# Optimization experiments

Measured on AMD Instinct MI355X. Metric: run time of the kernel, lower is better.

Reference implementation:

```python
import jax, jax.numpy as jnp
import numpy as np

N = 4            # polynomial nodes per segment
SEGMENTS = 32
IN_F = 1024
OUT_F = 1024
BATCH = 32
LENGTH = 2.0
HALF = 0.5 * LENGTH
K = (N - 1) * SEGMENTS + 1  # 97 coefficients per (out,in) pair


def setup_inputs() -> dict:
    key = jax.random.key(0)
    k1, k2 = jax.random.split(key)
    x = jax.random.uniform(k1, (BATCH, IN_F), jnp.float32, -1.0, 1.0)
    wm = 1.0 / IN_F  # uniform_(-weight_magnitude/in_features, +...)
    w = jax.random.uniform(k2, (OUT_F, IN_F, K), jnp.float32, -wm, wm)
    return {"x": x, "w": w}


def _lagrange_basis(x):
    # Chebyshev-Lobatto nodes on [-1, 1]: X_k = -cos(k*pi/(n-1))
    X = -jnp.cos(jnp.arange(N) * (np.pi / (N - 1))).astype(x.dtype)
    eye = jnp.eye(N, dtype=bool)
    D = jnp.where(eye, 1.0, X[:, None] - X[None, :])      # X[j] - X[m], diag -> 1
    diff = x[..., None, None] - X                          # [..., 1, n(m)]
    ratio = jnp.where(eye, 1.0, diff / D)                  # [..., n(j), n(m)]
    return jnp.prod(ratio, axis=-1)                        # [..., n] basis_j(x)


def reference(x, w):
    # segment index per element, clamped to [0, segments-1]
    id_min = jnp.clip(((x + HALF) / LENGTH * SEGMENTS).astype(jnp.int32), 0, SEGMENTS - 1)
    id_max = id_min + 1
    wid_min = id_min * (N - 1)                             # [B, I]
    idx = wid_min[..., None] + jnp.arange(N, dtype=jnp.int32)  # [B, I, n]
    # gather per-element coefficient windows: wsel[b,i,o,j] = w[o,i,idx[b,i,j]]
    w2 = jnp.transpose(w, (1, 0, 2))                       # [I, O, K]
    wsel = jnp.take_along_axis(w2[None], idx[:, :, None, :], axis=3)  # [B, I, O, n]
    # map x into local segment coordinates on [-half, half]
    x_min = 2.0 * id_min.astype(x.dtype) / SEGMENTS - 1.0
    x_max = 2.0 * id_max.astype(x.dtype) / SEGMENTS - 1.0
    x_in = LENGTH * (x - x_min) / (x_max - x_min) - HALF   # [B, I]
    basis = _lagrange_basis(x_in)                          # [B, I, n]
    # sum over in_features and nodes: 'ijk,jkli->jl' in the original repo
    return jnp.einsum('bin,bion->bo', basis, wsel)
```

## Files before the change

### kernel.cpp

```cpp
#include <hip/hip_runtime.h>

#define IN_F   1024
#define OUT_F  1024
#define KCOEF  97
#define CROWS  32
#define CFL    (CROWS * KCOEF)
#define CB     (CFL * 4)
#define NCH    32

typedef float f4 __attribute__((ext_vector_type(4)));

#define AS1 __attribute__((address_space(1)))
#define AS3 __attribute__((address_space(3)))

__global__ __launch_bounds__(256)
void pack_x(const float* __restrict__ x, float* __restrict__ xq) {
    int t = blockIdx.x * 256 + threadIdx.x;
    int b = t >> 10, i = t & 1023;
    xq[((i >> 2) << 7) + (b << 2) + (i & 3)] = x[t];
}

#define ISSUE_W(c, buf_) do {                                                   \
    const char* _gw = wbase + (size_t)(c) * CB;                                 \
    char* _lw = (char*)&shw[buf_][0];                                           \
    _Pragma("unroll")                                                           \
    for (int _k = 0; _k < 3; ++_k)                                              \
        __builtin_amdgcn_global_load_lds(                                       \
            (const AS1 void*)(_gw + (_k << 12) + (t << 4)),                     \
            (AS3 void*)(_lw + (_k << 12) + (wv << 10)), 16, 0, 0);              \
    if (lane < 2)                                                               \
        __builtin_amdgcn_global_load_lds(                                       \
            (const AS1 void*)(_gw + 12288 + (wv << 5) + (lane << 4)),           \
            (AS3 void*)(_lw + 12288 + (wv << 5)), 16, 0, 0);                    \
} while (0)

#define XLOAD(c) (*(const f4*)&xq[((((c) << 3) + g) << 7) + (b << 2)])

#define BASIS(b_, j_, xv_) do {                                           \
    _Pragma("unroll")                                                     \
    for (int _r = 0; _r < 4; ++_r) {                                      \
        float _x = xv_[_r];                                               \
        float _s = (_x + 1.0f) * 16.0f;                                   \
        int _id = (int)_s;                                                \
        _id = _id < 0 ? 0 : (_id > 31 ? 31 : _id);                        \
        float _d  = _x - ((float)_id * 0.0625f - 1.0f);                   \
        float _tt = fmaf(_d, 32.0f, -1.0f);                               \
        float _ap = _tt + 1.0f, _bp = _tt + 0.5f;                         \
        float _cm = _tt - 0.5f, _dm = _tt - 1.0f;                         \
        float _uu = _bp * _cm, _vv = _ap * _dm;                           \
        b_[_r][0] = _uu * _dm * (-2.0f / 3.0f);                           \
        b_[_r][1] = _vv * _cm * ( 4.0f / 3.0f);                           \
        b_[_r][2] = _vv * _bp * (-4.0f / 3.0f);                           \
        b_[_r][3] = _uu * _ap * ( 2.0f / 3.0f);                           \
        j_[_r] = _id * 3;                                                 \
    }                                                                     \
} while (0)

#define COMPUTE(b_, j_, buf_) do {                                        \
    const float* _rows = &shw[buf_][(g << 2) * KCOEF];                    \
    _Pragma("unroll")                                                     \
    for (int _r = 0; _r < 4; ++_r) {                                      \
        const float* _row = _rows + _r * KCOEF;                           \
        int _j = j_[_r];                                                  \
        float _w0 = _row[_j], _w1 = _row[_j + 1];                         \
        float _w2 = _row[_j + 2], _w3 = _row[_j + 3];                     \
        float _v = fmaf(b_[_r][0], _w0, fmaf(b_[_r][1], _w1,              \
                   fmaf(b_[_r][2], _w2, b_[_r][3] * _w3)));               \
        if (_r & 1) acc1 += _v; else acc0 += _v;                          \
    }                                                                     \
} while (0)

#define SBAR0() __builtin_amdgcn_sched_barrier(0)

#define WAITBAR(N) do {                                                   \
    asm volatile("s_waitcnt vmcnt(" #N ")" ::: "memory");                 \
    SBAR0();                                                              \
    __builtin_amdgcn_s_barrier();                                         \
    SBAR0();                                                              \
} while (0)

#define ENDBAR() do {                                                     \
    SBAR0();                                                              \
    __builtin_amdgcn_s_barrier();                                         \
    SBAR0();                                                              \
} while (0)

__global__ __launch_bounds__(256, 4)
void piecewise_main(const float* __restrict__ xq,
                    const float* __restrict__ w,
                    float* __restrict__ out) {
    const int bid = blockIdx.x;
    const int o = (bid & 7) * 128 + (bid >> 3);
    const int t    = threadIdx.x;
    const int wv   = t >> 6;
    const int lane = t & 63;
    const int g    = t >> 5;
    const int b    = t & 31;

    __shared__ __align__(16) float shw[3][CFL];
    __shared__ float red[256];

    const char* wbase = (const char*)(w + (size_t)o * (IN_F * KCOEF));

    float bA[4][4], bB[4][4];
    int   jA[4],   jB[4];
    float acc0 = 0.f, acc1 = 0.f;

    f4 xv0 = XLOAD(0);
    SBAR0();
    ISSUE_W(0, 0);
    ISSUE_W(1, 1);
    BASIS(bA, jA, xv0);

    for (int cc = 0; cc < 30; cc += 2) {
        const int p0 = cc % 3, p1 = (cc + 1) % 3, p2 = (cc + 2) % 3;
        f4 xv1 = XLOAD(cc + 1);
        SBAR0();
        ISSUE_W(cc + 2, p2);
        WAITBAR(4);
        BASIS(bB, jB, xv1);
        COMPUTE(bA, jA, p0);
        ENDBAR();
        f4 xv2 = XLOAD(cc + 2);
        SBAR0();
        ISSUE_W(cc + 3, p0);
        WAITBAR(4);
        BASIS(bA, jA, xv2);
        COMPUTE(bB, jB, p1);
        ENDBAR();
    }

    f4 xv31 = XLOAD(31);
    asm volatile("s_waitcnt vmcnt(0)" ::: "memory");
    SBAR0();
    __builtin_amdgcn_s_barrier();
    SBAR0();
    BASIS(bB, jB, xv31);
    COMPUTE(bA, jA, 0);
    COMPUTE(bB, jB, 1);

    red[t] = acc0 + acc1;
    __syncthreads();
    if (t < 32) {
        float sum = red[t];
        #pragma unroll
        for (int gg = 1; gg < 8; ++gg) sum += red[gg * 32 + t];
        out[t * OUT_F + o] = sum;
    }
}

extern "C" void kernel_launch(void* const* d_in, const int* in_sizes, int n_in,
                              void* d_out, int out_size, void* d_ws, size_t ws_size,
                              hipStream_t stream) {
    const float* x = (const float*)d_in[0];
    const float* w = (const float*)d_in[1];
    float*       out = (float*)d_out;
    float*       xq  = (float*)d_ws;

    pack_x<<<(32 * IN_F) / 256, 256, 0, stream>>>(x, xq);
    piecewise_main<<<OUT_F, 256, 0, stream>>>(xq, w, out);
}
```

Before: 80.72 us.

## Fuse x packing into main kernel and drop per-chunk end barrier

Removes the separate pack_x kernel and reads x directly from its row-major layout inside the main kernel, saving a launch and a workspace round trip. The triple-buffer loop is restructured with rotating LDS pointers and a single barrier per chunk instead of two, overlapping the next basis computation with outstanding loads. The direct x reads are less coalesced than the packed layout, and the single-barrier schedule depends on the vmcnt accounting being correct to avoid LDS races.

```diff
diff --git a/kernel.cpp b/kernel.cpp
--- a/kernel.cpp
+++ b/kernel.cpp
@@ -6,35 +6,28 @@
 #define CROWS  32
 #define CFL    (CROWS * KCOEF)
 #define CB     (CFL * 4)
-#define NCH    32
 
 typedef float f4 __attribute__((ext_vector_type(4)));
 
 #define AS1 __attribute__((address_space(1)))
 #define AS3 __attribute__((address_space(3)))
 
-__global__ __launch_bounds__(256)
-void pack_x(const float* __restrict__ x, float* __restrict__ xq) {
-    int t = blockIdx.x * 256 + threadIdx.x;
-    int b = t >> 10, i = t & 1023;
-    xq[((i >> 2) << 7) + (b << 2) + (i & 3)] = x[t];
-}
+#define SBAR0() __builtin_amdgcn_sched_barrier(0)
 
-#define ISSUE_W(c, buf_) do {                                                   \
-    const char* _gw = wbase + (size_t)(c) * CB;                                 \
-    char* _lw = (char*)&shw[buf_][0];                                           \
+#define ISSUE_W(c, lbuf) do {                                                   \
+    const char* _g = wbase + (size_t)(c) * CB;                                  \
     _Pragma("unroll")                                                           \
     for (int _k = 0; _k < 3; ++_k)                                              \
         __builtin_amdgcn_global_load_lds(                                       \
-            (const AS1 void*)(_gw + (_k << 12) + (t << 4)),                     \
-            (AS3 void*)(_lw + (_k << 12) + (wv << 10)), 16, 0, 0);              \
+            (const AS1 void*)(_g + (_k << 12) + (t << 4)),                      \
+            (AS3 void*)((lbuf) + (_k << 12) + (wv << 10)), 16, 0, 0);           \
     if (lane < 2)                                                               \
         __builtin_amdgcn_global_load_lds(                                       \
-            (const AS1 void*)(_gw + 12288 + (wv << 5) + (lane << 4)),           \
-            (AS3 void*)(_lw + 12288 + (wv << 5)), 16, 0, 0);                    \
+            (const AS1 void*)(_g + 12288 + (wv << 5) + (lane << 4)),            \
+            (AS3 void*)((lbuf) + 12288 + (wv << 5)), 16, 0, 0);                 \
 } while (0)
 
-#define XLOAD(c) (*(const f4*)&xq[((((c) << 3) + g) << 7) + (b << 2)])
+#define XLOAD(c) (*(const f4*)&xrow[((c) << 5) + (g << 2)])
 
 #define BASIS(b_, j_, xv_) do {                                           \
     _Pragma("unroll")                                                     \
@@ -56,8 +49,8 @@
     }                                                                     \
 } while (0)
 
-#define COMPUTE(b_, j_, buf_) do {                                        \
-    const float* _rows = &shw[buf_][(g << 2) * KCOEF];                    \
+#define COMPUTE(b_, j_, q_) do {                                          \
+    const float* _rows = (const float*)(q_) + (g << 2) * KCOEF;           \
     _Pragma("unroll")                                                     \
     for (int _r = 0; _r < 4; ++_r) {                                      \
         const float* _row = _rows + _r * KCOEF;                           \
@@ -70,8 +63,6 @@
     }                                                                     \
 } while (0)
 
-#define SBAR0() __builtin_amdgcn_sched_barrier(0)
-
 #define WAITBAR(N) do {                                                   \
     asm volatile("s_waitcnt vmcnt(" #N ")" ::: "memory");                 \
     SBAR0();                                                              \
@@ -79,16 +70,10 @@
     SBAR0();                                                              \
 } while (0)
 
-#define ENDBAR() do {                                                     \
-    SBAR0();                                                              \
-    __builtin_amdgcn_s_barrier();                                         \
-    SBAR0();                                                              \
-} while (0)
-
 __global__ __launch_bounds__(256, 4)
-void piecewise_main(const float* __restrict__ xq,
-                    const float* __restrict__ w,
-                    float* __restrict__ out) {
+void piecewise_fused(const float* __restrict__ x,
+                     const float* __restrict__ w,
+                     float* __restrict__ out) {
     const int bid = blockIdx.x;
     const int o = (bid & 7) * 128 + (bid >> 3);
     const int t    = threadIdx.x;
@@ -100,44 +85,46 @@
     __shared__ __align__(16) float shw[3][CFL];
     __shared__ float red[256];
 
-    const char* wbase = (const char*)(w + (size_t)o * (IN_F * KCOEF));
+    const char*  wbase = (const char*)(w + (size_t)o * (IN_F * KCOEF));
+    const float* xrow  = x + b * IN_F;
+
+    char* q0 = (char*)&shw[0][0];
+    char* q1 = (char*)&shw[1][0];
+    char* q2 = (char*)&shw[2][0];
 
     float bA[4][4], bB[4][4];
     int   jA[4],   jB[4];
+    f4 xvA, xvB;
     float acc0 = 0.f, acc1 = 0.f;
 
-    f4 xv0 = XLOAD(0);
-    SBAR0();
-    ISSUE_W(0, 0);
-    ISSUE_W(1, 1);
-    BASIS(bA, jA, xv0);
+    xvA = XLOAD(0);
+    BASIS(bA, jA, xvA);
+    ISSUE_W(0, q0);
+    xvB = XLOAD(1);
+    ISSUE_W(1, q1);
 
     for (int cc = 0; cc < 30; cc += 2) {
-        const int p0 = cc % 3, p1 = (cc + 1) % 3, p2 = (cc + 2) % 3;
-        f4 xv1 = XLOAD(cc + 1);
+        WAITBAR(6);
+        xvA = XLOAD(cc + 2);
+        ISSUE_W(cc + 2, q2);
+        COMPUTE(bA, jA, q0);
         SBAR0();
-        ISSUE_W(cc + 2, p2);
-        WAITBAR(4);
-        BASIS(bB, jB, xv1);
-        COMPUTE(bA, jA, p0);
-        ENDBAR();
-        f4 xv2 = XLOAD(cc + 2);
+        BASIS(bB, jB, xvB);
+        WAITBAR(6);
+        xvB = XLOAD(cc + 3);
+        ISSUE_W(cc + 3, q0);
+        COMPUTE(bB, jB, q1);
         SBAR0();
-        ISSUE_W(cc + 3, p0);
-        WAITBAR(4);
-        BASIS(bA, jA, xv2);
-        COMPUTE(bB, jB, p1);
-        ENDBAR();
+        BASIS(bA, jA, xvA);
+        char* tmp = q0; q0 = q2; q2 = q1; q1 = tmp;
     }
 
-    f4 xv31 = XLOAD(31);
-    asm volatile("s_waitcnt vmcnt(0)" ::: "memory");
+    WAITBAR(6);
+    COMPUTE(bA, jA, q0);
     SBAR0();
-    __builtin_amdgcn_s_barrier();
-    SBAR0();
-    BASIS(bB, jB, xv31);
-    COMPUTE(bA, jA, 0);
-    COMPUTE(bB, jB, 1);
+    BASIS(bB, jB, xvB);
+    WAITBAR(0);
+    COMPUTE(bB, jB, q1);
 
     red[t] = acc0 + acc1;
     __syncthreads();
@@ -155,8 +142,5 @@
     const float* x = (const float*)d_in[0];
     const float* w = (const float*)d_in[1];
     float*       out = (float*)d_out;
-    float*       xq  = (float*)d_ws;
-
-    pack_x<<<(32 * IN_F) / 256, 256, 0, stream>>>(x, xq);
-    piecewise_main<<<OUT_F, 256, 0, stream>>>(xq, w, out);
+    piecewise_fused<<<OUT_F, 256, 0, stream>>>(x, w, out);
 }
```

After: 75.66 us. -6.3%, faster.
